# Kernel optimization log

Measured on AMD Instinct MI355X. Metric: run time of the kernel, lower is better.

Reference implementation:

```python
import jax, jax.numpy as jnp
import numpy as np

D_MODEL = 2048
D_INNER = 4096
D_CONV = 4
D_STATE = 16
DT_RANK = 128  # (d_model + 15) // 16
EPS = 1e-5
B_SZ, SEQ = 2, 2048


def _silu(x):
    return x * jax.nn.sigmoid(x)


def setup_inputs() -> dict:
    key = jax.random.key(0)
    ks = jax.random.split(key, 10)
    s = lambda k, shape, sc=0.02: jax.random.normal(k, shape, jnp.float32) * sc
    # S4D-real init for A_log, small negative bias for dt (standard Mamba init)
    A_log = jnp.log(jnp.tile(jnp.arange(1, D_STATE + 1, dtype=jnp.float32), (D_INNER, 1)))
    return {
        "hidden_states": jax.random.normal(ks[0], (B_SZ, SEQ, D_MODEL), jnp.float32),
        "norm_scale": jnp.ones((D_MODEL,), jnp.float32),
        "in_proj_w": s(ks[1], (2 * D_INNER, D_MODEL)),
        "conv_w": s(ks[2], (D_INNER, 1, D_CONV), 0.1),
        "conv_b": s(ks[3], (D_INNER,), 0.1),
        "x_proj_w": s(ks[4], (DT_RANK + 2 * D_STATE, D_INNER)),
        "dt_proj_w": s(ks[5], (D_INNER, DT_RANK), 0.1),
        "dt_proj_b": jnp.full((D_INNER,), -4.0, jnp.float32) + s(ks[6], (D_INNER,), 0.1),
        "out_proj_w": s(ks[7], (D_MODEL, D_INNER)),
        "A_log": A_log,
        "D": jnp.ones((D_INNER,), jnp.float32),
    }


def reference(hidden_states, norm_scale, in_proj_w, conv_w, conv_b, x_proj_w,
              dt_proj_w, dt_proj_b, out_proj_w, A_log, D):
    B, L, _ = hidden_states.shape
    residual = hidden_states
    # RMSNorm
    rms = jnp.sqrt(jnp.mean(hidden_states ** 2, axis=-1, keepdims=True) + EPS)
    xn = hidden_states / rms * norm_scale
    # in_proj -> [B, L, 2*d_inner]; torch code keeps this as projected_states
    xz = jnp.einsum('bld,ed->ble', xn, in_proj_w)
    x_in = xz[..., :D_INNER].transpose(0, 2, 1)  # [B, d_inner, L]
    z = xz[..., D_INNER:]                        # [B, L, d_inner]
    # depthwise causal conv1d (padding d_conv-1, truncated to L) + SiLU
    xc = jax.lax.conv_general_dilated(
        x_in, conv_w, window_strides=(1,), padding=[(D_CONV - 1, 0)],
        feature_group_count=D_INNER)
    xc = _silu(xc + conv_b[None, :, None])       # [B, d_inner, L]
    # x_proj -> dt, B, C
    x_dbl = jnp.einsum('bdl,rd->brl', xc, x_proj_w)  # [B, dt_rank+2*d_state, L]
    dt_low = x_dbl[:, :DT_RANK]
    Bm = x_dbl[:, DT_RANK:DT_RANK + D_STATE]         # [B, d_state, L]
    Cm = x_dbl[:, DT_RANK + D_STATE:]                # [B, d_state, L]
    delta = jax.nn.softplus(
        jnp.einsum('dr,brl->bdl', dt_proj_w, dt_low) + dt_proj_b[None, :, None])
    A = -jnp.exp(A_log)                              # [d_inner, d_state]
    # selective scan: h_t = exp(delta_t * A) * h_{t-1} + delta_t * B_t * u_t
    delta_t = delta.transpose(2, 0, 1)  # [L, B, d_inner]
    u_t = xc.transpose(2, 0, 1)         # [L, B, d_inner]
    B_t = Bm.transpose(2, 0, 1)         # [L, B, d_state]
    C_t = Cm.transpose(2, 0, 1)         # [L, B, d_state]

    def step(h, inp):
        d_, b_, c_, u_ = inp
        dA = jnp.exp(d_[..., None] * A)                      # [B, d_inner, d_state]
        h = h * dA + (d_ * u_)[..., None] * b_[:, None, :]   # [B, d_inner, d_state]
        y = jnp.einsum('bds,bs->bd', h, c_)                  # [B, d_inner]
        return h, y

    h0 = jnp.zeros((B, D_INNER, D_STATE), hidden_states.dtype)
    _, ys = jax.lax.scan(step, h0, (delta_t, B_t, C_t, u_t))  # [L, B, d_inner]
    y = ys.transpose(1, 0, 2) + xc.transpose(0, 2, 1) * D     # [B, L, d_inner]
    y = y * _silu(z)
    out = jnp.einsum('bld,od->blo', y, out_proj_w)            # [B, L, d_model]
    return residual + out, xz
```

## Files before the change

kernel.cpp:

```cpp
#include <hip/hip_runtime.h>
#include <cstdint>
#include <cstddef>

#define DM   2048
#define DI   4096
#define DST  16
#define DTR  128
#define SEQL 2048
#define NTOK 4096
#define XZW  8192
#define NCHAIN 8192
#define CL   32
#define NCH  64

typedef short short8 __attribute__((ext_vector_type(8)));
typedef float f32x4 __attribute__((ext_vector_type(4)));

__device__ __forceinline__ short f2bf(float x) {
  union { float f; uint32_t u; } v; v.f = x;
  uint32_t r = v.u + 0x7fffu + ((v.u >> 16) & 1u);
  return (short)(r >> 16);
}
__device__ __forceinline__ float bf2f(short s) {
  union { uint32_t u; float f; } v; v.u = ((uint32_t)(uint16_t)s) << 16;
  return v.f;
}

__device__ __forceinline__ void stage16(const short* g, short* l) {
#if __has_builtin(__builtin_amdgcn_global_load_lds)
  __builtin_amdgcn_global_load_lds((const __attribute__((address_space(1))) void*)g,
                                   (__attribute__((address_space(3))) void*)l, 16, 0, 0);
#else
  *(short8*)l = *(const short8*)g;
#endif
}

__global__ __launch_bounds__(256) void cvt4_k(const float* __restrict__ in,
                                              short* __restrict__ out, int n4) {
  int i = blockIdx.x * 256 + threadIdx.x;
  if (i >= n4) return;
  float4 v = ((const float4*)in)[i];
  short4 o;
  o.x = f2bf(v.x); o.y = f2bf(v.y); o.z = f2bf(v.z); o.w = f2bf(v.w);
  ((short4*)out)[i] = o;
}

__global__ __launch_bounds__(256) void pad_xproj_k(const float* __restrict__ xp,
                                                   short* __restrict__ out) {
  int i = blockIdx.x * 256 + threadIdx.x;
  if (i >= 256 * 1024) return;
  int r = i >> 10;
  float4 v = make_float4(0.f, 0.f, 0.f, 0.f);
  if (r < 160) v = ((const float4*)xp)[i];
  short4 o;
  o.x = f2bf(v.x); o.y = f2bf(v.y); o.z = f2bf(v.z); o.w = f2bf(v.w);
  ((short4*)out)[i] = o;
}

__global__ __launch_bounds__(256) void rmsnorm_k(const float* __restrict__ hs,
                                                 const float* __restrict__ sc,
                                                 short* __restrict__ xn) {
  const int token = blockIdx.x;
  const int tid = threadIdx.x;
  const float* row = hs + (size_t)token * DM;
  float4 a = ((const float4*)row)[tid];
  float4 b = ((const float4*)row)[tid + 256];
  float ss = a.x*a.x + a.y*a.y + a.z*a.z + a.w*a.w
           + b.x*b.x + b.y*b.y + b.z*b.z + b.w*b.w;
  #pragma unroll
  for (int o = 32; o > 0; o >>= 1) ss += __shfl_xor(ss, o);
  __shared__ float wsum[4];
  if ((tid & 63) == 0) wsum[tid >> 6] = ss;
  __syncthreads();
  float tot = wsum[0] + wsum[1] + wsum[2] + wsum[3];
  float inv = rsqrtf(tot * (1.0f / DM) + 1e-5f);
  float4 s1 = ((const float4*)sc)[tid];
  float4 s2 = ((const float4*)sc)[tid + 256];
  short4 o1, o2;
  o1.x = f2bf(a.x * inv * s1.x); o1.y = f2bf(a.y * inv * s1.y);
  o1.z = f2bf(a.z * inv * s1.z); o1.w = f2bf(a.w * inv * s1.w);
  o2.x = f2bf(b.x * inv * s2.x); o2.y = f2bf(b.y * inv * s2.y);
  o2.z = f2bf(b.z * inv * s2.z); o2.w = f2bf(b.w * inv * s2.w);
  ((short4*)xn)[(size_t)token * (DM / 4) + tid] = o1;
  ((short4*)xn)[(size_t)token * (DM / 4) + tid + 256] = o2;
}

#define LGKM_FENCE() do { asm volatile("s_waitcnt lgkmcnt(0)" ::: "memory"); \
                          __builtin_amdgcn_sched_barrier(0); } while (0)

template <int MFR, int EPI, int RBY, int RBX>
__global__ __launch_bounds__(512) void gemm_big(const short* __restrict__ A,
                                                const short* __restrict__ B,
                                                int K, int N, int nbx,
                                                float* __restrict__ out_f,
                                                const float* __restrict__ aux_f) {
  constexpr int BM = MFR * 32;
  constexpr int ABYTES = BM * 128;
  constexpr int BBYTES = 256 * 128;
  constexpr int AINSTR = ABYTES / 8192;
  constexpr int BUF = ABYTES + BBYTES;
  constexpr int FPP = MFR / 2;
  __shared__ char lds[2 * BUF];

  const int tid = threadIdx.x;
  const int lane = tid & 63;
  const int wid = tid >> 6;
  const int wm = wid >> 2;
  const int wn = wid & 3;
  const int lr = lane & 15;
  const int lj = lane >> 4;

  const int xcd = blockIdx.x & 7;
  const int idx = blockIdx.x >> 3;
  const int nrgx = nbx / RBX;
  const int by = (xcd / nrgx) * RBY + idx / RBX;
  const int bx = (xcd % nrgx) * RBX + idx % RBX;
  const size_t m0 = (size_t)by * BM;
  const size_t n0 = (size_t)bx * 256;

  const int NT = K >> 6;

  auto stA1 = [&](int t, char* buf, int s) {
    const int k0 = t << 6;
    const int off = s * 8192 + tid * 16;
    const int r = off >> 7;
    const int j = (off >> 4) & 7;
    stage16(A + (m0 + r) * (size_t)K + k0 + ((j ^ (r & 7)) << 3),
            (short*)(buf + off));
  };
  auto stB1 = [&](int t, char* buf, int s) {
    const int k0 = t << 6;
    const int off = s * 8192 + tid * 16;
    const int r = off >> 7;
    const int j = (off >> 4) & 7;
    stage16(B + (n0 + r) * (size_t)K + k0 + ((j ^ (r & 7)) << 3),
            (short*)(buf + ABYTES + off));
  };

#define READ_A(dst, fbase)                                                   \
  _Pragma("unroll")                                                          \
  for (int f = 0; f < 4; ++f) {                                              \
    const int arow = wm * (BM / 2) + ((fbase) + f) * 16 + lr;                \
    _Pragma("unroll")                                                        \
    for (int ks = 0; ks < 2; ++ks)                                           \
      dst[f][ks] = *(const short8*)(cur + arow * 128 +                       \
                     ((((ks << 2) + lj) ^ (arow & 7)) << 4));                \
  }
#define READ_B(dst, gbase)                                                   \
  _Pragma("unroll")                                                          \
  for (int g = 0; g < 2; ++g) {                                              \
    const int brow = wn * 64 + ((gbase) + g) * 16 + lr;                      \
    _Pragma("unroll")                                                        \
    for (int ks = 0; ks < 2; ++ks)                                           \
      dst[g][ks] = *(const short8*)(cur + ABYTES + brow * 128 +              \
                     ((((ks << 2) + lj) ^ (brow & 7)) << 4));                \
  }
#define MFMA_Q(accoff, avoff, gbase, bvx)                                    \
  __builtin_amdgcn_s_setprio(1);                                             \
  _Pragma("unroll")                                                          \
  for (int ks = 0; ks < 2; ++ks)                                             \
    _Pragma("unroll")                                                        \
    for (int f = 0; f < FPP; ++f)                                            \
      _Pragma("unroll")                                                      \
      for (int g = 0; g < 2; ++g)                                            \
        acc[(accoff) + f][(gbase) + g] = __builtin_amdgcn_mfma_f32_16x16x32_bf16( \
            av[(avoff) + f][ks], bvx[g][ks], acc[(accoff) + f][(gbase) + g], 0, 0, 0); \
  __builtin_amdgcn_s_setprio(0);

  f32x4 acc[MFR][4] = {};

  {
    #pragma unroll
    for (int s = 0; s < AINSTR; ++s) stA1(0, lds, s);
    #pragma unroll
    for (int s = 0; s < 4; ++s) stB1(0, lds, s);
    if constexpr (MFR == 8) {
      if (NT > 1) {
        stA1(1, lds + BUF, 0); stA1(1, lds + BUF, 2);
        asm volatile("s_waitcnt vmcnt(2)" ::: "memory");
      } else asm volatile("s_waitcnt vmcnt(0)" ::: "memory");
    } else {
      if (NT > 1) {
        stA1(1, lds + BUF, 0);
        asm volatile("s_waitcnt vmcnt(1)" ::: "memory");
      } else asm volatile("s_waitcnt vmcnt(0)" ::: "memory");
    }
    __builtin_amdgcn_s_barrier();
    __builtin_amdgcn_sched_barrier(0);
  }

  for (int t = 0; t < NT; ++t) {
    char* cur = lds + (t & 1) * BUF;
    char* nxt = lds + ((t + 1) & 1) * BUF;
    const bool m1 = (t + 1) < NT;
    const bool m2 = (t + 2) < NT;
    short8 av[4][2], bv0[2][2], bv1[2][2];

    if constexpr (MFR == 8) {
      READ_A(av, 0);
      READ_B(bv0, 0);
      if (m1) { stA1(t + 1, nxt, 1); stA1(t + 1, nxt, 3); }
      LGKM_FENCE();
      MFMA_Q(0, 0, 0, bv0);
      __builtin_amdgcn_s_barrier();

      READ_B(bv1, 2);
      if (m1) { stB1(t + 1, nxt, 0); stB1(t + 1, nxt, 1); }
      LGKM_FENCE();
      MFMA_Q(0, 0, 2, bv1);
      __builtin_amdgcn_s_barrier();

      READ_A(av, 4);
      if (m1) { stB1(t + 1, nxt, 2); stB1(t + 1, nxt, 3); }
      if (m2) { stA1(t + 2, cur, 0); stA1(t + 2, cur, 2); }
      LGKM_FENCE();
      MFMA_Q(4, 0, 2, bv1);
      __builtin_amdgcn_s_barrier();

      MFMA_Q(4, 0, 0, bv0);
      if (m2) asm volatile("s_waitcnt vmcnt(2)" ::: "memory");
      else    asm volatile("s_waitcnt vmcnt(0)" ::: "memory");
      __builtin_amdgcn_s_barrier();
      __builtin_amdgcn_sched_barrier(0);
    } else {
      READ_A(av, 0);
      READ_B(bv0, 0);
      if (m1) stA1(t + 1, nxt, 1);
      LGKM_FENCE();
      MFMA_Q(0, 0, 0, bv0);
      __builtin_amdgcn_s_barrier();

      READ_B(bv1, 2);
      if (m1) { stB1(t + 1, nxt, 0); stB1(t + 1, nxt, 1); }
      LGKM_FENCE();
      MFMA_Q(0, 0, 2, bv1);
      __builtin_amdgcn_s_barrier();

      if (m1) { stB1(t + 1, nxt, 2); stB1(t + 1, nxt, 3); }
      if (m2) stA1(t + 2, cur, 0);
      MFMA_Q(2, 2, 2, bv1);
      __builtin_amdgcn_s_barrier();

      MFMA_Q(2, 2, 0, bv0);
      if (m2) asm volatile("s_waitcnt vmcnt(1)" ::: "memory");
      else    asm volatile("s_waitcnt vmcnt(0)" ::: "memory");
      __builtin_amdgcn_s_barrier();
      __builtin_amdgcn_sched_barrier(0);
    }
  }

  #pragma unroll
  for (int f = 0; f < MFR; ++f)
    #pragma unroll
    for (int g = 0; g < 4; ++g)
      #pragma unroll
      for (int jj = 0; jj < 4; ++jj) {
        const size_t row = m0 + wm * (BM / 2) + f * 16 + lj * 4 + jj;
        const size_t col = n0 + wn * 64 + g * 16 + lr;
        float v = acc[f][g][jj];
        if constexpr (EPI == 3) v += aux_f[row * (size_t)N + col];
        out_f[row * (size_t)N + col] = v;
      }
#undef READ_A
#undef READ_B
#undef MFMA_Q
}

template <int EPI>
__global__ __launch_bounds__(256) void gemm_nt(const short* __restrict__ A,
                                               const short* __restrict__ B,
                                               int ld, int K, int N,
                                               float* __restrict__ out_f,
                                               const float* __restrict__ aux_f,
                                               short* __restrict__ out_bf) {
  __shared__ short As[128 * 64];
  __shared__ short Bs[128 * 64];
  const int tid = threadIdx.x;
  const int lane = tid & 63;
  const int wid = tid >> 6;
  const int wr = wid >> 1, wc = wid & 1;
  const size_t m0 = (size_t)blockIdx.y * 128;
  const size_t n0 = (size_t)blockIdx.x * 128;
  A += (size_t)blockIdx.z * K;
  B += (size_t)blockIdx.z * K;
  f32x4 acc[4][4] = {};
  for (int k0 = 0; k0 < K; k0 += 64) {
    #pragma unroll
    for (int i = 0; i < 4; ++i) {
      const int off = i * 4096 + tid * 16;
      const int r = off >> 7;
      const int ke = (off & 127) >> 1;
      stage16(A + (m0 + r) * (size_t)ld + k0 + ke, &As[off >> 1]);
      stage16(B + (n0 + r) * (size_t)ld + k0 + ke, &Bs[off >> 1]);
    }
    __syncthreads();
    #pragma unroll
    for (int kk = 0; kk < 64; kk += 32) {
      short8 af[4], bfr[4];
      const int kb = kk + (lane >> 4) * 8;
      const int rr = lane & 15;
      #pragma unroll
      for (int f = 0; f < 4; ++f) {
        af[f]  = *(const short8*)&As[(wr * 64 + f * 16 + rr) * 64 + kb];
        bfr[f] = *(const short8*)&Bs[(wc * 64 + f * 16 + rr) * 64 + kb];
      }
      #pragma unroll
      for (int fm = 0; fm < 4; ++fm)
        #pragma unroll
        for (int fn = 0; fn < 4; ++fn)
          acc[fm][fn] = __builtin_amdgcn_mfma_f32_16x16x32_bf16(af[fm], bfr[fn], acc[fm][fn], 0, 0, 0);
    }
    __syncthreads();
  }
  const int rbase = (lane >> 4) * 4;
  const int cbase = lane & 15;
  #pragma unroll
  for (int fm = 0; fm < 4; ++fm) {
    #pragma unroll
    for (int fn = 0; fn < 4; ++fn) {
      #pragma unroll
      for (int j = 0; j < 4; ++j) {
        const size_t row = m0 + wr * 64 + fm * 16 + rbase + j;
        const size_t col = n0 + wc * 64 + fn * 16 + cbase;
        const float v = acc[fm][fn][j];
        if constexpr (EPI == 2) {
          float x = v + aux_f[col];
          float sp = (x > 20.f) ? x : log1pf(__expf(x));
          out_bf[row * (size_t)N + col] = f2bf(sp);
        } else {
          if (col < 160)
            out_f[((size_t)blockIdx.z * NTOK + row) * (size_t)N + col] = v;
        }
      }
    }
  }
}

__global__ __launch_bounds__(256) void xdbl_epi_k(const float* __restrict__ part,
                                                  short* __restrict__ dtl,
                                                  float* __restrict__ Bc,
                                                  float* __restrict__ Cc) {
  const int row = blockIdx.x;
  const int col = threadIdx.x;
  if (col >= 160) return;
  const size_t i = (size_t)row * 256 + col;
  const float v = part[i] + part[(size_t)NTOK * 256 + i]
                + part[(size_t)2 * NTOK * 256 + i]
                + part[(size_t)3 * NTOK * 256 + i];
  if (col < 128)      dtl[(size_t)row * 128 + col] = f2bf(v);
  else if (col < 144) Bc[(size_t)row * 16 + (col - 128)] = v;
  else                Cc[(size_t)row * 16 + (col - 144)] = v;
}

__global__ __launch_bounds__(256) void conv_silu_k(const float* __restrict__ xz,
                                                   const float* __restrict__ cw,
                                                   const float* __restrict__ cb,
                                                   short* __restrict__ xc) {
  const int d = blockIdx.x * 256 + threadIdx.x;
  const int t0 = blockIdx.y * 8;
  const int l0 = t0 & (SEQL - 1);
  const float4 w = ((const float4*)cw)[d];
  const float bias = cb[d];
  float x0 = (l0 >= 3) ? xz[(size_t)(t0 - 3) * XZW + d] : 0.f;
  float x1 = (l0 >= 2) ? xz[(size_t)(t0 - 2) * XZW + d] : 0.f;
  float x2 = (l0 >= 1) ? xz[(size_t)(t0 - 1) * XZW + d] : 0.f;
  #pragma unroll
  for (int i = 0; i < 8; ++i) {
    const float x3 = xz[(size_t)(t0 + i) * XZW + d];
    const float acc = bias + w.x * x0 + w.y * x1 + w.z * x2 + w.w * x3;
    const float sv = acc / (1.f + __expf(-acc));
    xc[(size_t)(t0 + i) * DI + d] = f2bf(sv);
    x0 = x1; x1 = x2; x2 = x3;
  }
}

__global__ __launch_bounds__(256) void scan1_k(const short* __restrict__ del_bf,
                                               const short* __restrict__ xc,
                                               const float* __restrict__ Bc,
                                               const float* __restrict__ alog,
                                               float* __restrict__ hloc,
                                               float* __restrict__ Ssum) {
  const int t = blockIdx.x * 256 + threadIdx.x;
  const int sub = t & 1;
  const int chain = (t >> 1) & (NCHAIN - 1);
  const int chunk = t >> 14;
  const int b = chain >> 12;
  const int d = chain & 4095;
  float A[8];
  #pragma unroll
  for (int j = 0; j < 8; ++j) A[j] = -__expf(alog[d * 16 + sub * 8 + j]);
  float h[8] = {};
  float S = 0.f;
  size_t token = (size_t)b * SEQL + (size_t)chunk * CL;
  #pragma unroll 2
  for (int l = 0; l < CL; ++l, ++token) {
    const float delta = bf2f(del_bf[token * DI + d]);
    const float u = bf2f(xc[token * DI + d]);
    const float du = delta * u;
    S += delta;
    const float4 B0 = ((const float4*)Bc)[token * 4 + sub * 2];
    const float4 B1 = ((const float4*)Bc)[token * 4 + sub * 2 + 1];
    const float Bv[8] = {B0.x, B0.y, B0.z, B0.w, B1.x, B1.y, B1.z, B1.w};
    #pragma unroll
    for (int j = 0; j < 8; ++j)
      h[j] = h[j] * __expf(delta * A[j]) + du * Bv[j];
  }
  const size_t idx = (size_t)(chunk * NCHAIN + chain) * 4 + sub * 2;
  ((float4*)hloc)[idx]     = make_float4(h[0], h[1], h[2], h[3]);
  ((float4*)hloc)[idx + 1] = make_float4(h[4], h[5], h[6], h[7]);
  if (sub == 0) Ssum[chunk * NCHAIN + chain] = S;
}

__global__ __launch_bounds__(256) void scan2_k(float* __restrict__ hloc,
                                               const float* __restrict__ Ssum,
                                               const float* __restrict__ alog) {
  const int t = blockIdx.x * 256 + threadIdx.x;
  const int q = t & 3;
  const int chain = t >> 2;
  const int d = chain & 4095;
  float A[4];
  #pragma unroll
  for (int j = 0; j < 4; ++j) A[j] = -__expf(alog[d * 16 + q * 4 + j]);
  float4 h = make_float4(0.f, 0.f, 0.f, 0.f);
  for (int c = 0; c < NCH; ++c) {
    const size_t idx = (size_t)(c * NCHAIN + chain) * 4 + q;
    const float S = Ssum[c * NCHAIN + chain];
    const float4 hl = ((const float4*)hloc)[idx];
    ((float4*)hloc)[idx] = h;
    h.x = h.x * __expf(A[0] * S) + hl.x;
    h.y = h.y * __expf(A[1] * S) + hl.y;
    h.z = h.z * __expf(A[2] * S) + hl.z;
    h.w = h.w * __expf(A[3] * S) + hl.w;
  }
}

__global__ __launch_bounds__(256) void scan3_k(const short* __restrict__ del_bf,
                                               const short* __restrict__ xc,
                                               const float* __restrict__ Bc,
                                               const float* __restrict__ Cc,
                                               const float* __restrict__ xzbuf,
                                               const float* __restrict__ alog,
                                               const float* __restrict__ dvec,
                                               const float* __restrict__ hin,
                                               short* __restrict__ y) {
  const int t = blockIdx.x * 256 + threadIdx.x;
  const int sub = t & 1;
  const int chain = (t >> 1) & (NCHAIN - 1);
  const int chunk = t >> 14;
  const int b = chain >> 12;
  const int d = chain & 4095;
  float A[8];
  #pragma unroll
  for (int j = 0; j < 8; ++j) A[j] = -__expf(alog[d * 16 + sub * 8 + j]);
  const float Dd = dvec[d];
  const size_t idx = (size_t)(chunk * NCHAIN + chain) * 4 + sub * 2;
  const float4 h0 = ((const float4*)hin)[idx];
  const float4 h1 = ((const float4*)hin)[idx + 1];
  float h[8] = {h0.x, h0.y, h0.z, h0.w, h1.x, h1.y, h1.z, h1.w};
  size_t token = (size_t)b * SEQL + (size_t)chunk * CL;
  #pragma unroll 2
  for (int l = 0; l < CL; ++l, ++token) {
    const float delta = bf2f(del_bf[token * DI + d]);
    const float u = bf2f(xc[token * DI + d]);
    const float du = delta * u;
    const float4 B0 = ((const float4*)Bc)[token * 4 + sub * 2];
    const float4 B1 = ((const float4*)Bc)[token * 4 + sub * 2 + 1];
    const float4 C0 = ((const float4*)Cc)[token * 4 + sub * 2];
    const float4 C1 = ((const float4*)Cc)[token * 4 + sub * 2 + 1];
    const float Bv[8] = {B0.x, B0.y, B0.z, B0.w, B1.x, B1.y, B1.z, B1.w};
    const float Cv[8] = {C0.x, C0.y, C0.z, C0.w, C1.x, C1.y, C1.z, C1.w};
    float yp = 0.f;
    #pragma unroll
    for (int j = 0; j < 8; ++j) {
      h[j] = h[j] * __expf(delta * A[j]) + du * Bv[j];
      yp += h[j] * Cv[j];
    }
    yp += __shfl_xor(yp, 1);
    if (sub == 0) {
      const float z = xzbuf[token * XZW + DI + d];
      const float sz = z / (1.f + __expf(-z));
      y[token * DI + d] = f2bf((yp + u * Dd) * sz);
    }
  }
}

extern "C" void kernel_launch(void* const* d_in, const int* in_sizes, int n_in,
                              void* d_out, int out_size, void* d_ws, size_t ws_size,
                              hipStream_t stream) {
  const float* hs   = (const float*)d_in[0];
  const float* nsc  = (const float*)d_in[1];
  const float* win  = (const float*)d_in[2];
  const float* cw   = (const float*)d_in[3];
  const float* cb   = (const float*)d_in[4];
  const float* wxp  = (const float*)d_in[5];
  const float* wdt  = (const float*)d_in[6];
  const float* bdt  = (const float*)d_in[7];
  const float* wout = (const float*)d_in[8];
  const float* alog = (const float*)d_in[9];
  const float* dvec = (const float*)d_in[10];

  float* out0 = (float*)d_out;
  float* xz   = out0 + (size_t)NTOK * DM;

  char* w = (char*)d_ws;
  size_t off = 0;
  auto alloc = [&](size_t bytes) {
    char* p = w + off;
    off += (bytes + 255) & ~(size_t)255;
    return p;
  };
  short* xn_bf   = (short*)alloc((size_t)NTOK * DM * 2);
  short* win_bf  = (short*)alloc((size_t)XZW * DM * 2);
  short* wout_bf = (short*)alloc((size_t)DM * DI * 2);
  short* wdt_bf  = (short*)alloc((size_t)DI * DTR * 2);
  short* wxp_bf  = (short*)alloc((size_t)256 * DI * 2);
  short* xc_bf   = (short*)alloc((size_t)NTOK * DI * 2);
  short* dtl_bf  = (short*)alloc((size_t)NTOK * DTR * 2);
  float* Bc      = (float*)alloc((size_t)NTOK * DST * 4);
  float* Cc      = (float*)alloc((size_t)NTOK * DST * 4);
  short* del_bf  = (short*)alloc((size_t)NTOK * DI * 2);
  short* y_bf    = (short*)alloc((size_t)NTOK * DI * 2);

  float* xp_part = (float*)win_bf;
  float* hloc    = (float*)win_bf;
  float* Ssum    = (float*)xn_bf;

  cvt4_k<<<16384, 256, 0, stream>>>(win,  win_bf,  (XZW * DM) / 4);
  cvt4_k<<<8192,  256, 0, stream>>>(wout, wout_bf, (DM * DI) / 4);
  cvt4_k<<<512,   256, 0, stream>>>(wdt,  wdt_bf,  (DI * DTR) / 4);
  pad_xproj_k<<<1024, 256, 0, stream>>>(wxp, wxp_bf);

  rmsnorm_k<<<NTOK, 256, 0, stream>>>(hs, nsc, xn_bf);
  gemm_big<8, 0, 8, 8><<<dim3((XZW / 256) * (NTOK / 256)), 512, 0, stream>>>(
      xn_bf, win_bf, DM, XZW, XZW / 256, xz, nullptr);
  conv_silu_k<<<dim3(DI / 256, NTOK / 8), 256, 0, stream>>>(xz, cw, cb, xc_bf);
  gemm_nt<4><<<dim3(2, NTOK / 128, 4), 256, 0, stream>>>(
      xc_bf, wxp_bf, DI, DI / 4, 256, xp_part, nullptr, nullptr);
  xdbl_epi_k<<<NTOK, 256, 0, stream>>>(xp_part, dtl_bf, Bc, Cc);
  gemm_nt<2><<<dim3(DI / 128, NTOK / 128, 1), 256, 0, stream>>>(
      dtl_bf, wdt_bf, DTR, DTR, DI, nullptr, bdt, del_bf);
  scan1_k<<<(NCHAIN * 2 * NCH) / 256, 256, 0, stream>>>(
      del_bf, xc_bf, Bc, alog, hloc, Ssum);
  scan2_k<<<(NCHAIN * 4) / 256, 256, 0, stream>>>(hloc, Ssum, alog);
  scan3_k<<<(NCHAIN * 2 * NCH) / 256, 256, 0, stream>>>(
      del_bf, xc_bf, Bc, Cc, xz, alog, dvec, hloc, y_bf);
  gemm_big<4, 3, 8, 4><<<dim3((DM / 256) * (NTOK / 128)), 512, 0, stream>>>(
      y_bf, wout_bf, DI, DM, DM / 256, out0, hs);
}
```

Before: 567.8 us.

## Use split-K with 256x256 tiles for out_proj GEMM plus combine kernel

The out_proj GEMM previously used 128x256 tiles with a fused residual add. It now uses the larger 256x256 tile path, splitting K into two halves across blockIdx.y to keep the block count at 256. Each half writes fp32 partials into a reused scratch buffer, and a new combine kernel adds the two partials and the residual. Larger tiles are meant to raise arithmetic intensity per block. In exchange, the change adds a 2x fp32 partial write and read through memory plus an extra kernel launch.

Result: no change. 560.6 us (-1.3%).

```diff
diff --git a/kernel.cpp b/kernel.cpp
--- a/kernel.cpp
+++ b/kernel.cpp
@@ -88,18 +88,18 @@
 #define LGKM_FENCE() do { asm volatile("s_waitcnt lgkmcnt(0)" ::: "memory"); \
                           __builtin_amdgcn_sched_barrier(0); } while (0)
 
-template <int MFR, int EPI, int RBY, int RBX>
+template <int RBY, int RBX>
 __global__ __launch_bounds__(512) void gemm_big(const short* __restrict__ A,
                                                 const short* __restrict__ B,
-                                                int K, int N, int nbx,
+                                                int K, int ksz, int N, int nbx,
                                                 float* __restrict__ out_f,
-                                                const float* __restrict__ aux_f) {
-  constexpr int BM = MFR * 32;
+                                                size_t zstride) {
+  constexpr int MFR = 8;
+  constexpr int BM = 256;
   constexpr int ABYTES = BM * 128;
   constexpr int BBYTES = 256 * 128;
-  constexpr int AINSTR = ABYTES / 8192;
   constexpr int BUF = ABYTES + BBYTES;
-  constexpr int FPP = MFR / 2;
+  constexpr int FPP = 4;
   __shared__ char lds[2 * BUF];
 
   const int tid = threadIdx.x;
@@ -118,10 +118,12 @@
   const size_t m0 = (size_t)by * BM;
   const size_t n0 = (size_t)bx * 256;
 
-  const int NT = K >> 6;
+  const int kbase = blockIdx.y * ksz;
+  out_f += (size_t)blockIdx.y * zstride;
+  const int NT = ksz >> 6;
 
   auto stA1 = [&](int t, char* buf, int s) {
-    const int k0 = t << 6;
+    const int k0 = kbase + (t << 6);
     const int off = s * 8192 + tid * 16;
     const int r = off >> 7;
     const int j = (off >> 4) & 7;
@@ -129,7 +131,7 @@
             (short*)(buf + off));
   };
   auto stB1 = [&](int t, char* buf, int s) {
-    const int k0 = t << 6;
+    const int k0 = kbase + (t << 6);
     const int off = s * 8192 + tid * 16;
     const int r = off >> 7;
     const int j = (off >> 4) & 7;
@@ -171,20 +173,13 @@
 
   {
     #pragma unroll
-    for (int s = 0; s < AINSTR; ++s) stA1(0, lds, s);
+    for (int s = 0; s < 4; ++s) stA1(0, lds, s);
     #pragma unroll
     for (int s = 0; s < 4; ++s) stB1(0, lds, s);
-    if constexpr (MFR == 8) {
-      if (NT > 1) {
-        stA1(1, lds + BUF, 0); stA1(1, lds + BUF, 2);
-        asm volatile("s_waitcnt vmcnt(2)" ::: "memory");
-      } else asm volatile("s_waitcnt vmcnt(0)" ::: "memory");
-    } else {
-      if (NT > 1) {
-        stA1(1, lds + BUF, 0);
-        asm volatile("s_waitcnt vmcnt(1)" ::: "memory");
-      } else asm volatile("s_waitcnt vmcnt(0)" ::: "memory");
-    }
+    if (NT > 1) {
+      stA1(1, lds + BUF, 0); stA1(1, lds + BUF, 2);
+      asm volatile("s_waitcnt vmcnt(2)" ::: "memory");
+    } else asm volatile("s_waitcnt vmcnt(0)" ::: "memory");
     __builtin_amdgcn_s_barrier();
     __builtin_amdgcn_sched_barrier(0);
   }
@@ -196,57 +191,31 @@
     const bool m2 = (t + 2) < NT;
     short8 av[4][2], bv0[2][2], bv1[2][2];
 
-    if constexpr (MFR == 8) {
-      READ_A(av, 0);
-      READ_B(bv0, 0);
-      if (m1) { stA1(t + 1, nxt, 1); stA1(t + 1, nxt, 3); }
-      LGKM_FENCE();
-      MFMA_Q(0, 0, 0, bv0);
-      __builtin_amdgcn_s_barrier();
-
-      READ_B(bv1, 2);
-      if (m1) { stB1(t + 1, nxt, 0); stB1(t + 1, nxt, 1); }
-      LGKM_FENCE();
-      MFMA_Q(0, 0, 2, bv1);
-      __builtin_amdgcn_s_barrier();
-
-      READ_A(av, 4);
-      if (m1) { stB1(t + 1, nxt, 2); stB1(t + 1, nxt, 3); }
-      if (m2) { stA1(t + 2, cur, 0); stA1(t + 2, cur, 2); }
-      LGKM_FENCE();
-      MFMA_Q(4, 0, 2, bv1);
-      __builtin_amdgcn_s_barrier();
-
-      MFMA_Q(4, 0, 0, bv0);
-      if (m2) asm volatile("s_waitcnt vmcnt(2)" ::: "memory");
-      else    asm volatile("s_waitcnt vmcnt(0)" ::: "memory");
-      __builtin_amdgcn_s_barrier();
-      __builtin_amdgcn_sched_barrier(0);
-    } else {
-      READ_A(av, 0);
-      READ_B(bv0, 0);
-      if (m1) stA1(t + 1, nxt, 1);
-      LGKM_FENCE();
-      MFMA_Q(0, 0, 0, bv0);
-      __builtin_amdgcn_s_barrier();
-
-      READ_B(bv1, 2);
-      if (m1) { stB1(t + 1, nxt, 0); stB1(t + 1, nxt, 1); }
-      LGKM_FENCE();
-      MFMA_Q(0, 0, 2, bv1);
-      __builtin_amdgcn_s_barrier();
-
-      if (m1) { stB1(t + 1, nxt, 2); stB1(t + 1, nxt, 3); }
-      if (m2) stA1(t + 2, cur, 0);
-      MFMA_Q(2, 2, 2, bv1);
-      __builtin_amdgcn_s_barrier();
-
-      MFMA_Q(2, 2, 0, bv0);
-      if (m2) asm volatile("s_waitcnt vmcnt(1)" ::: "memory");
-      else    asm volatile("s_waitcnt vmcnt(0)" ::: "memory");
-      __builtin_amdgcn_s_barrier();
-      __builtin_amdgcn_sched_barrier(0);
-    }
+    READ_A(av, 0);
+    READ_B(bv0, 0);
+    if (m1) { stA1(t + 1, nxt, 1); stA1(t + 1, nxt, 3); }
+    LGKM_FENCE();
+    MFMA_Q(0, 0, 0, bv0);
+    __builtin_amdgcn_s_barrier();
+
+    READ_B(bv1, 2);
+    if (m1) { stB1(t + 1, nxt, 0); stB1(t + 1, nxt, 1); }
+    LGKM_FENCE();
+    MFMA_Q(0, 0, 2, bv1);
+    __builtin_amdgcn_s_barrier();
+
+    READ_A(av, 4);
+    if (m1) { stB1(t + 1, nxt, 2); stB1(t + 1, nxt, 3); }
+    if (m2) { stA1(t + 2, cur, 0); stA1(t + 2, cur, 2); }
+    LGKM_FENCE();
+    MFMA_Q(4, 0, 2, bv1);
+    __builtin_amdgcn_s_barrier();
+
+    MFMA_Q(4, 0, 0, bv0);
+    if (m2) asm volatile("s_waitcnt vmcnt(2)" ::: "memory");
+    else    asm volatile("s_waitcnt vmcnt(0)" ::: "memory");
+    __builtin_amdgcn_s_barrier();
+    __builtin_amdgcn_sched_barrier(0);
   }
 
   #pragma unroll
@@ -257,13 +226,24 @@
       for (int jj = 0; jj < 4; ++jj) {
         const size_t row = m0 + wm * (BM / 2) + f * 16 + lj * 4 + jj;
         const size_t col = n0 + wn * 64 + g * 16 + lr;
-        float v = acc[f][g][jj];
-        if constexpr (EPI == 3) v += aux_f[row * (size_t)N + col];
-        out_f[row * (size_t)N + col] = v;
+        out_f[row * (size_t)N + col] = acc[f][g][jj];
       }
 #undef READ_A
 #undef READ_B
 #undef MFMA_Q
+}
+
+__global__ __launch_bounds__(256) void combine_k(const float* __restrict__ part,
+                                                 const float* __restrict__ hs,
+                                                 float* __restrict__ out0) {
+  const size_t i = (size_t)blockIdx.x * 256 + threadIdx.x;
+  const float4 p0 = ((const float4*)part)[i];
+  const float4 p1 = ((const float4*)part)[i + (size_t)NTOK * DM / 4];
+  const float4 r  = ((const float4*)hs)[i];
+  float4 o;
+  o.x = r.x + p0.x + p1.x; o.y = r.y + p0.y + p1.y;
+  o.z = r.z + p0.z + p1.z; o.w = r.w + p0.w + p1.w;
+  ((float4*)out0)[i] = o;
 }
 
 template <int EPI>
@@ -524,6 +504,7 @@
   float* xp_part = (float*)win_bf;
   float* hloc    = (float*)win_bf;
   float* Ssum    = (float*)xn_bf;
+  float* opart   = (float*)xc_bf;
 
   cvt4_k<<<16384, 256, 0, stream>>>(win,  win_bf,  (XZW * DM) / 4);
   cvt4_k<<<8192,  256, 0, stream>>>(wout, wout_bf, (DM * DI) / 4);
@@ -531,8 +512,8 @@
   pad_xproj_k<<<1024, 256, 0, stream>>>(wxp, wxp_bf);
 
   rmsnorm_k<<<NTOK, 256, 0, stream>>>(hs, nsc, xn_bf);
-  gemm_big<8, 0, 8, 8><<<dim3((XZW / 256) * (NTOK / 256)), 512, 0, stream>>>(
-      xn_bf, win_bf, DM, XZW, XZW / 256, xz, nullptr);
+  gemm_big<8, 8><<<dim3((XZW / 256) * (NTOK / 256)), 512, 0, stream>>>(
+      xn_bf, win_bf, DM, DM, XZW, XZW / 256, xz, 0);
   conv_silu_k<<<dim3(DI / 256, NTOK / 8), 256, 0, stream>>>(xz, cw, cb, xc_bf);
   gemm_nt<4><<<dim3(2, NTOK / 128, 4), 256, 0, stream>>>(
       xc_bf, wxp_bf, DI, DI / 4, 256, xp_part, nullptr, nullptr);
@@ -544,6 +525,7 @@
   scan2_k<<<(NCHAIN * 4) / 256, 256, 0, stream>>>(hloc, Ssum, alog);
   scan3_k<<<(NCHAIN * 2 * NCH) / 256, 256, 0, stream>>>(
       del_bf, xc_bf, Bc, Cc, xz, alog, dvec, hloc, y_bf);
-  gemm_big<4, 3, 8, 4><<<dim3((DM / 256) * (NTOK / 128)), 512, 0, stream>>>(
-      y_bf, wout_bf, DI, DM, DM / 256, out0, hs);
-}
+  gemm_big<4, 4><<<dim3((DM / 256) * (NTOK / 256), 2), 512, 0, stream>>>(
+      y_bf, wout_bf, DI, DI / 2, DM, DM / 256, opart, (size_t)NTOK * DM);
+  combine_k<<<(NTOK * DM / 4) / 256, 256, 0, stream>>>(opart, hs, out0);
+}
```
